# Optimization experiments

Measured on AMD Instinct MI355X. Metric: run time of the kernel, lower is better.

The kernel has to match this reference:

```python
import jax, jax.numpy as jnp
import numpy as np

KERNEL_SIZE = 7      # odd, per assert in __init__
MAX_VAL = 1e4        # kornia morphology default max_val


def setup_inputs() -> dict:
    key = jax.random.key(0)
    kx, ka, kb, kc = jax.random.split(key, 4)
    x = jax.random.normal(kx, (8, 64, 256, 256), dtype=jnp.float32)
    k1 = jax.random.uniform(ka, (1,), dtype=jnp.float32)
    k2 = jax.random.uniform(kb, (1,), dtype=jnp.float32)
    k3 = jax.random.uniform(kc, (1,), dtype=jnp.float32)
    return {"x": x, "k1": k1, "k2": k2, "k3": k3}


def _structuring_element(k1, k2, k3):
    k = KERNEL_SIZE
    # torch.arange(-k//2 + 1, k//2 + 1) with floor-div == -(k//2)..k//2 for odd k
    c = jnp.arange(-(k // 2), k // 2 + 1, dtype=jnp.float32)
    xg, yg = jnp.meshgrid(c, c, indexing='xy')
    se = k1[0] * xg ** 2 + 2.0 * k2[0] * xg * yg + k3[0] * yg ** 2
    se = se / se.max()
    return -se  # (k, k)


def reference(x, k1, k2, k3):
    k = KERNEL_SIZE
    se = _structuring_element(k1, k2, k3)
    # flat kernel of ones with center zeroed -> center tap masked to -max_val
    mask = np.ones((k, k), dtype=bool)
    mask[k // 2, k // 2] = False
    neighborhood = jnp.where(jnp.asarray(mask), se, -MAX_VAL)
    nb = neighborhood[::-1, ::-1]  # kornia dilation flips the neighborhood

    pad = k // 2
    # geodesic border for dilation: pad with -max_val
    xp = jnp.pad(x, ((0, 0), (0, 0), (pad, pad), (pad, pad)),
                 constant_values=-MAX_VAL)
    H, W = x.shape[-2], x.shape[-1]
    # fused running max over the k*k taps; avoids materializing the unfold
    out = jnp.full_like(x, -jnp.inf)
    for i in range(k):
        for j in range(k):
            out = jnp.maximum(out, xp[..., i:i + H, j:j + W] + nb[i, j])
    return out
```

## Files before the change

### kernel.cpp

```cpp
#include <hip/hip_runtime.h>


#define MAXV 10000.0f

constexpr int H = 256;
constexpr int W = 256;

typedef float vf4 __attribute__((ext_vector_type(4)));
typedef float vf2 __attribute__((ext_vector_type(2)));

__global__ __launch_bounds__(256, 4) void morpho_kernel(
    const float* __restrict__ x,
    const float* __restrict__ k1p,
    const float* __restrict__ k2p,
    const float* __restrict__ k3p,
    float* __restrict__ out) {
  const int tid = threadIdx.x;
  const int lane = tid & 63;
  const int wid = __builtin_amdgcn_readfirstlane(tid >> 6);
  const int p = blockIdx.x >> 2;
  const int y0w = (blockIdx.x & 3) * 64 + wid * 16;

  const float* __restrict__ xp = x + (size_t)p * (H * W);
  float* __restrict__ op = out + (size_t)p * (H * W);

  const float k1v = k1p[0], k2v = k2p[0], k3v = k3p[0];
  const int ia = lane >> 3, ib = lane & 7;
  const float xg = (float)(((ib < 6) ? ib : 6) - 3);
  const float yg = (float)(((ia < 6) ? ia : 6) - 3);
  const float sev = k1v * (xg * xg) + 2.0f * k2v * (xg * yg) + k3v * (yg * yg);
  float mx = sev;
#pragma unroll
  for (int off = 32; off; off >>= 1) mx = fmaxf(mx, __shfl_xor(mx, off, 64));
  const float wv = 0.0f - sev * (1.0f / mx);

  vf2 wp[7][3];
  float w6[7];
#pragma unroll
  for (int d = 0; d < 7; ++d) {
#pragma unroll
    for (int m = 0; m < 3; ++m) {
      vf2 pr;
      pr.x = __int_as_float(__builtin_amdgcn_readlane(__float_as_int(wv), d * 8 + 2 * m));
      pr.y = __int_as_float(__builtin_amdgcn_readlane(__float_as_int(wv), d * 8 + 2 * m + 1));
      wp[d][m] = pr;
    }
    w6[d] = __int_as_float(__builtin_amdgcn_readlane(__float_as_int(wv), d * 8 + 6));
  }
  wp[3][1].y = -MAXV;

  const bool l0 = (lane == 0);
  const bool l63 = (lane == 63);
  const int o1 = lane * 4;
  const int o0 = l0 ? o1 : o1 - 4;
  const int o2 = l63 ? o1 : o1 + 4;

  vf4 ring[3][3];
  {
    const int r0 = (y0w - 3 < 0) ? 0 : y0w - 3;
    const float* __restrict__ rb = xp + r0 * W;
    ring[0][0] = *reinterpret_cast<const vf4*>(rb + o0);
    ring[0][1] = *reinterpret_cast<const vf4*>(rb + o1);
    ring[0][2] = *reinterpret_cast<const vf4*>(rb + o2);
  }
  {
    const int r1 = (y0w - 2 < 0) ? 0 : y0w - 2;
    const float* __restrict__ rb = xp + r1 * W;
    ring[1][0] = *reinterpret_cast<const vf4*>(rb + o0);
    ring[1][1] = *reinterpret_cast<const vf4*>(rb + o1);
    ring[1][2] = *reinterpret_cast<const vf4*>(rb + o2);
  }

  float acc[7][4];
#pragma unroll
  for (int s = 0; s < 7; ++s)
#pragma unroll
    for (int c = 0; c < 4; ++c) acc[s][c] = -INFINITY;

#pragma unroll
  for (int iy = 0; iy < 22; ++iy) {
    if (iy < 20) {
      int rp = y0w - 1 + iy;
      rp = (rp < 0) ? 0 : ((rp > H - 1) ? H - 1 : rp);
      const float* __restrict__ rb = xp + rp * W;
      const int sl = (iy + 2) % 3;
      ring[sl][0] = *reinterpret_cast<const vf4*>(rb + o0);
      ring[sl][1] = *reinterpret_cast<const vf4*>(rb + o1);
      ring[sl][2] = *reinterpret_cast<const vf4*>(rb + o2);
    }

    const int r = y0w - 3 + iy;
    if ((iy >= 3 && iy <= 18) || (r >= 0 && r < H)) {
      const int cs = iy % 3;
      vf4 q0 = ring[cs][0];
      vf4 q1 = ring[cs][1];
      vf4 q2 = ring[cs][2];

      q0.y = l0 ? -MAXV : q0.y;
      q0.z = l0 ? -MAXV : q0.z;
      q0.w = l0 ? -MAXV : q0.w;
      q2.x = l63 ? -MAXV : q2.x;
      q2.y = l63 ? -MAXV : q2.y;
      q2.z = l63 ? -MAXV : q2.z;

      const vf2 O0 = __builtin_shufflevector(q0, q0, 1, 2);
      const vf2 O1 = __builtin_shufflevector(q0, q1, 3, 4);
      const vf2 O2 = __builtin_shufflevector(q1, q1, 1, 2);
      const vf2 O3 = __builtin_shufflevector(q1, q2, 3, 4);
      const vf2 E0 = __builtin_shufflevector(q0, q0, 2, 3);
      const vf2 E1 = __builtin_shufflevector(q1, q1, 0, 1);
      const vf2 E2 = __builtin_shufflevector(q1, q1, 2, 3);
      const vf2 E3 = __builtin_shufflevector(q2, q2, 0, 1);

      const vf2 P[4][3] = {{O0, O1, O2}, {E0, E1, E2}, {O1, O2, O3}, {E1, E2, E3}};
      const float T[4] = {q1.w, q2.x, q2.y, q2.z};

#pragma unroll
      for (int dd = 0; dd < 7; ++dd) {
        const int t = iy - dd;
        if (t < 0 || t > 15) continue;
        const int st = t % 7;
#pragma unroll
        for (int c = 0; c < 4; ++c) {
          const vf2 a = P[c][0] + wp[dd][0];
          const vf2 b = P[c][1] + wp[dd][1];
          const vf2 g = P[c][2] + wp[dd][2];
          const float s6 = T[c] + w6[dd];
          const float m0 = fmaxf(fmaxf(a.x, a.y), b.x);
          const float m1 = fmaxf(fmaxf(b.y, g.x), g.y);
          const float m2 = fmaxf(fmaxf(s6, m0), m1);
          acc[st][c] = fmaxf(acc[st][c], m2);
        }
      }
    }

    if (iy >= 6) {
      const int tr = iy - 6;
      const int st = tr % 7;
      vf4 v;
      v.x = acc[st][0];
      v.y = acc[st][1];
      v.z = acc[st][2];
      v.w = acc[st][3];
      __builtin_nontemporal_store(
          v, reinterpret_cast<vf4*>(&op[(y0w + tr) * W + o1]));
      if (iy <= 14) {
#pragma unroll
        for (int c = 0; c < 4; ++c) acc[st][c] = -INFINITY;
      }
    }
  }
}

extern "C" void kernel_launch(void* const* d_in, const int* in_sizes, int n_in,
                              void* d_out, int out_size, void* d_ws, size_t ws_size,
                              hipStream_t stream) {
  const float* x = (const float*)d_in[0];
  const float* k1 = (const float*)d_in[1];
  const float* k2 = (const float*)d_in[2];
  const float* k3 = (const float*)d_in[3];
  float* outp = (float*)d_out;

  const int planes = 8 * 64;
  const int blocks = planes * 4;
  morpho_kernel<<<dim3(blocks), dim3(256), 0, stream>>>(x, k1, k2, k3, outp);
}
```

Before: 249.4 us.

## Halve rows per wave and fetch horizontal halo via lane shuffles

Each wave now produces 8 output rows instead of 16, so twice as many blocks are launched, and occupancy is raised to 6 blocks per SIMD. The per-lane neighbour vectors used to be loaded from global memory with three vf4 loads per row; they are now built from a single load plus cross-lane shuffles, which also removes the three-slot register ring. The aim is more parallelism and lower register and load pressure. The cost is a larger vertical halo overhead (14 rows read per 8 written instead of 22 per 16) and extra shuffle instructions.

```diff
diff --git a/kernel.cpp b/kernel.cpp
--- a/kernel.cpp
+++ b/kernel.cpp
@@ -9,7 +9,7 @@
 typedef float vf4 __attribute__((ext_vector_type(4)));
 typedef float vf2 __attribute__((ext_vector_type(2)));
 
-__global__ __launch_bounds__(256, 4) void morpho_kernel(
+__global__ __launch_bounds__(256, 6) void morpho_kernel(
     const float* __restrict__ x,
     const float* __restrict__ k1p,
     const float* __restrict__ k2p,
@@ -18,8 +18,8 @@
   const int tid = threadIdx.x;
   const int lane = tid & 63;
   const int wid = __builtin_amdgcn_readfirstlane(tid >> 6);
-  const int p = blockIdx.x >> 2;
-  const int y0w = (blockIdx.x & 3) * 64 + wid * 16;
+  const int p = blockIdx.x >> 3;
+  const int y0w = ((blockIdx.x & 7) * 4 + wid) * 8;
 
   const float* __restrict__ xp = x + (size_t)p * (H * W);
   float* __restrict__ op = out + (size_t)p * (H * W);
@@ -52,24 +52,6 @@
   const bool l0 = (lane == 0);
   const bool l63 = (lane == 63);
   const int o1 = lane * 4;
-  const int o0 = l0 ? o1 : o1 - 4;
-  const int o2 = l63 ? o1 : o1 + 4;
-
-  vf4 ring[3][3];
-  {
-    const int r0 = (y0w - 3 < 0) ? 0 : y0w - 3;
-    const float* __restrict__ rb = xp + r0 * W;
-    ring[0][0] = *reinterpret_cast<const vf4*>(rb + o0);
-    ring[0][1] = *reinterpret_cast<const vf4*>(rb + o1);
-    ring[0][2] = *reinterpret_cast<const vf4*>(rb + o2);
-  }
-  {
-    const int r1 = (y0w - 2 < 0) ? 0 : y0w - 2;
-    const float* __restrict__ rb = xp + r1 * W;
-    ring[1][0] = *reinterpret_cast<const vf4*>(rb + o0);
-    ring[1][1] = *reinterpret_cast<const vf4*>(rb + o1);
-    ring[1][2] = *reinterpret_cast<const vf4*>(rb + o2);
-  }
 
   float acc[7][4];
 #pragma unroll
@@ -78,23 +60,21 @@
     for (int c = 0; c < 4; ++c) acc[s][c] = -INFINITY;
 
 #pragma unroll
-  for (int iy = 0; iy < 22; ++iy) {
-    if (iy < 20) {
-      int rp = y0w - 1 + iy;
-      rp = (rp < 0) ? 0 : ((rp > H - 1) ? H - 1 : rp);
-      const float* __restrict__ rb = xp + rp * W;
-      const int sl = (iy + 2) % 3;
-      ring[sl][0] = *reinterpret_cast<const vf4*>(rb + o0);
-      ring[sl][1] = *reinterpret_cast<const vf4*>(rb + o1);
-      ring[sl][2] = *reinterpret_cast<const vf4*>(rb + o2);
-    }
+  for (int iy = 0; iy < 14; ++iy) {
+    const int r = y0w - 3 + iy;
+    const int rc = (r < 0) ? 0 : ((r > H - 1) ? H - 1 : r);
+    const vf4 q1 = *reinterpret_cast<const vf4*>(xp + rc * W + o1);
 
-    const int r = y0w - 3 + iy;
-    if ((iy >= 3 && iy <= 18) || (r >= 0 && r < H)) {
-      const int cs = iy % 3;
-      vf4 q0 = ring[cs][0];
-      vf4 q1 = ring[cs][1];
-      vf4 q2 = ring[cs][2];
+    if ((iy >= 3 && iy <= 10) || (r >= 0 && r < H)) {
+      vf4 q0, q2;
+      q0.x = q1.x;
+      q0.y = __shfl_up(q1.y, 1, 64);
+      q0.z = __shfl_up(q1.z, 1, 64);
+      q0.w = __shfl_up(q1.w, 1, 64);
+      q2.x = __shfl_down(q1.x, 1, 64);
+      q2.y = __shfl_down(q1.y, 1, 64);
+      q2.z = __shfl_down(q1.z, 1, 64);
+      q2.w = q1.w;
 
       q0.y = l0 ? -MAXV : q0.y;
       q0.z = l0 ? -MAXV : q0.z;
@@ -118,7 +98,7 @@
 #pragma unroll
       for (int dd = 0; dd < 7; ++dd) {
         const int t = iy - dd;
-        if (t < 0 || t > 15) continue;
+        if (t < 0 || t > 7) continue;
         const int st = t % 7;
 #pragma unroll
         for (int c = 0; c < 4; ++c) {
@@ -144,7 +124,7 @@
       v.w = acc[st][3];
       __builtin_nontemporal_store(
           v, reinterpret_cast<vf4*>(&op[(y0w + tr) * W + o1]));
-      if (iy <= 14) {
+      if (iy == 6) {
 #pragma unroll
         for (int c = 0; c < 4; ++c) acc[st][c] = -INFINITY;
       }
@@ -162,6 +142,6 @@
   float* outp = (float*)d_out;
 
   const int planes = 8 * 64;
-  const int blocks = planes * 4;
+  const int blocks = planes * 8;
   morpho_kernel<<<dim3(blocks), dim3(256), 0, stream>>>(x, k1, k2, k3, outp);
 }
```

Result: no change. 248.7 us (-0.3%).
